# Kernel tuning notes

Measured on AMD Instinct MI355X. Metric: run time of the kernel, lower is better.

The kernel has to match this reference:

```python
import jax, jax.numpy as jnp
import numpy as np

LATENT_DIM = 64
CONTEXT_DIM = 128
NUM_LAYERS = 5
NUM_BINS = 8
HIDDEN = 256
TAIL_BOUND = 5.0
MIN_BIN_W = 1e-3
MIN_BIN_H = 1e-3
MIN_DERIV = 1e-3
BATCH = 32768


def setup_inputs() -> dict:
    key = jax.random.key(0)
    ks = jax.random.split(key, 8)
    D, C, L, H = LATENT_DIM, CONTEXT_DIM, NUM_LAYERS, HIDDEN
    out_dim = D * (3 * NUM_BINS - 1)  # 64*23 = 1472
    n_tri = D * (D - 1) // 2  # 2016
    s = 0.05
    return {
        "inputs": jax.random.normal(ks[0], (BATCH, D), jnp.float32) * 2.0,
        "context": jax.random.normal(ks[1], (BATCH, C), jnp.float32),
        "W1": jax.random.normal(ks[2], (L, C, H), jnp.float32) * s,
        "b1": jnp.zeros((L, H), jnp.float32),
        "W2": jax.random.normal(ks[3], (L, H, H), jnp.float32) * s,
        "b2": jnp.zeros((L, H), jnp.float32),
        "W3": jax.random.normal(ks[4], (L, H, out_dim), jnp.float32) * s,
        "b3": jnp.zeros((L, out_dim), jnp.float32),
        "lu_bias": jnp.zeros((L, D), jnp.float32),
        "lower_entries": jax.random.normal(ks[5], (L, n_tri), jnp.float32) * s,
        "upper_entries": jax.random.normal(ks[6], (L, n_tri), jnp.float32) * s,
        "upper_diag": jax.random.normal(ks[7], (L, D), jnp.float32) * s,
    }


def _unconstrained_rqs(x, uw, uh, ud):
    """Rational-quadratic spline with linear tails (nflows semantics).
    x: [B, D]; uw/uh: [B, D, NUM_BINS]; ud: [B, D, NUM_BINS-1].
    Returns (y [B,D], logabsdet [B,D])."""
    Bnd = TAIL_BOUND
    nb = NUM_BINS
    inside = (x >= -Bnd) & (x <= Bnd)
    # pad unnormalized derivatives so boundary derivative == 1
    const = float(np.log(np.exp(1.0 - MIN_DERIV) - 1.0))
    ud = jnp.pad(ud, ((0, 0), (0, 0), (1, 1)), constant_values=const)  # [B,D,nb+1]

    w = jax.nn.softmax(uw, axis=-1)
    w = MIN_BIN_W + (1.0 - MIN_BIN_W * nb) * w
    cumw = jnp.concatenate(
        [jnp.zeros(w.shape[:-1] + (1,), w.dtype), jnp.cumsum(w, axis=-1)], axis=-1)
    cumw = 2.0 * Bnd * cumw - Bnd
    cumw = cumw.at[..., 0].set(-Bnd).at[..., -1].set(Bnd)
    widths = cumw[..., 1:] - cumw[..., :-1]

    h = jax.nn.softmax(uh, axis=-1)
    h = MIN_BIN_H + (1.0 - MIN_BIN_H * nb) * h
    cumh = jnp.concatenate(
        [jnp.zeros(h.shape[:-1] + (1,), h.dtype), jnp.cumsum(h, axis=-1)], axis=-1)
    cumh = 2.0 * Bnd * cumh - Bnd
    cumh = cumh.at[..., 0].set(-Bnd).at[..., -1].set(Bnd)
    heights = cumh[..., 1:] - cumh[..., :-1]

    derivs = MIN_DERIV + jax.nn.softplus(ud)  # [B,D,nb+1]
    delta = heights / widths                  # [B,D,nb]

    xc = jnp.clip(x, -Bnd, Bnd)
    # searchsorted: sum(x >= bin_edges) - 1, clipped to valid bin range
    idx = jnp.clip(jnp.sum(xc[..., None] >= cumw, axis=-1) - 1, 0, nb - 1)[..., None]
    g = lambda a: jnp.take_along_axis(a, idx, axis=-1)[..., 0]

    in_cw = g(cumw)
    in_w = g(widths)
    in_ch = g(cumh)
    in_h = g(heights)
    in_delta = g(delta)
    in_d = g(derivs)
    in_d1 = g(derivs[..., 1:])

    theta = (xc - in_cw) / in_w
    tomt = theta * (1.0 - theta)
    numer = in_h * (in_delta * theta * theta + in_d * tomt)
    denom = in_delta + (in_d + in_d1 - 2.0 * in_delta) * tomt
    out = in_ch + numer / denom
    dnum = in_delta * in_delta * (
        in_d1 * theta * theta + 2.0 * in_delta * tomt + in_d * (1.0 - theta) ** 2)
    ld = jnp.log(dnum) - 2.0 * jnp.log(denom)

    return jnp.where(inside, out, x), jnp.where(inside, ld, 0.0)


def _lu_forward(x, lower_e, upper_e, udiag, bias):
    """nflows LULinear: y = L @ (U @ x) + b, logabsdet = sum(log diag(U))."""
    D = x.shape[-1]
    li = jnp.tril_indices(D, -1)
    ui = jnp.triu_indices(D, 1)
    Lm = jnp.eye(D, dtype=x.dtype).at[li].set(lower_e)
    diag = jax.nn.softplus(udiag) + 1e-3
    Um = jnp.zeros((D, D), x.dtype).at[ui].set(upper_e) + jnp.diag(diag)
    y = x @ Um.T
    y = y @ Lm.T + bias
    return y, jnp.sum(jnp.log(diag))


def reference(inputs, context, W1, b1, W2, b2, W3, b3,
              lu_bias, lower_entries, upper_entries, upper_diag):
    x = inputs
    logdet = jnp.zeros(x.shape[0], x.dtype)
    for l in range(NUM_LAYERS):
        # conditioning net (mask=ones => net sees only context)
        hh = jax.nn.relu(context @ W1[l] + b1[l])
        hh = jax.nn.relu(hh @ W2[l] + b2[l])
        params = (hh @ W3[l] + b3[l]).reshape(x.shape[0], LATENT_DIM, 3 * NUM_BINS - 1)
        uw = params[..., :NUM_BINS]
        uh = params[..., NUM_BINS:2 * NUM_BINS]
        ud = params[..., 2 * NUM_BINS:]
        x, ld = _unconstrained_rqs(x, uw, uh, ud)
        logdet = logdet + jnp.sum(ld, axis=-1)
        x, lld = _lu_forward(x, lower_entries[l], upper_entries[l],
                             upper_diag[l], lu_bias[l])
        logdet = logdet + lld
    base = -0.5 * jnp.sum(x * x, axis=-1) - 0.5 * LATENT_DIM * float(np.log(2.0 * np.pi))
    return base + logdet
```

## Files before the change

kernel.cpp:

```cpp
#include <hip/hip_runtime.h>
#include <hip/hip_bf16.h>
#include <math.h>

#define D 64
#define CDIM 128
#define NL 5
#define NB 8
#define HID 256
#define ODIM 1472
#define PPD 23
#define PPDP 24
#define NPAD 1536
#define NTRI 2016
#define BATCH 32768
#define CHUNK 8192

typedef unsigned short u16;
typedef __attribute__((ext_vector_type(8))) short bf16x8;
typedef __attribute__((ext_vector_type(8))) unsigned short u16x8;
typedef __attribute__((ext_vector_type(4))) float f32x4;
typedef __attribute__((ext_vector_type(8))) float f32x8;

__device__ __forceinline__ float softplusf(float x) {
    return fmaxf(x, 0.0f) + log1pf(__expf(-fabsf(x)));
}
__device__ __forceinline__ float softplus_fast(float x) {
    return fmaxf(x, 0.0f) + __logf(1.0f + __expf(-fabsf(x)));
}
__device__ __forceinline__ float frcp(float x) { return __builtin_amdgcn_rcpf(x); }
__device__ __forceinline__ u16 f2bf(float f) {
    __hip_bfloat16 h = __float2bfloat16(f);
    return *reinterpret_cast<u16*>(&h);
}
__device__ __forceinline__ float bf2f(u16 u) {
    return __uint_as_float(((unsigned int)u) << 16);
}

__device__ __forceinline__ void gload16(const u16* g, const u16* s) {
    __builtin_amdgcn_global_load_lds(
        (const __attribute__((address_space(1))) unsigned int*)(unsigned long long)(uintptr_t)g,
        (__attribute__((address_space(3))) unsigned int*)(unsigned int)(uintptr_t)s,
        16, 0, 0);
}

__device__ __forceinline__ int xcd_swz(int bid, int nwg) {
    int q = nwg >> 3, r = nwg & 7;
    int xcd = bid & 7, idx = bid >> 3;
    return (xcd < r ? xcd * (q + 1) : r * (q + 1) + (xcd - r) * q) + idx;
}

__global__ void cvt_ctx(const float* __restrict__ c, u16* __restrict__ o) {
    int i = blockIdx.x * 256 + threadIdx.x;
    if (i < BATCH * CDIM / 4) {
        float4 v = reinterpret_cast<const float4*>(c)[i];
        unsigned lo = (unsigned)f2bf(v.x) | ((unsigned)f2bf(v.y) << 16);
        unsigned hi = (unsigned)f2bf(v.z) | ((unsigned)f2bf(v.w) << 16);
        uint2 pv; pv.x = lo; pv.y = hi;
        reinterpret_cast<uint2*>(o)[i] = pv;
    }
}

template<int MAP>
__global__ __launch_bounds__(256) void transpose_prep(
    const float* __restrict__ in, u16* __restrict__ out, int R, int C, int Cout)
{
    __shared__ u16 tile[32][33];
    const int l = blockIdx.z;
    const int c0 = blockIdx.x * 32, r0 = blockIdx.y * 32;
    const int tx = threadIdx.x & 31, ty = threadIdx.x >> 5;
    const float* inl = in + (size_t)l * R * C;
#pragma unroll
    for (int i = 0; i < 4; ++i) {
        int r = r0 + ty * 4 + i;
        int cc = c0 + tx;
        int src = cc;
        if (MAP) { int dd = cc / PPDP, pp = cc % PPDP; src = (pp < PPD) ? dd * PPD + pp : -1; }
        u16 v = 0;
        if (src >= 0) v = f2bf(inl[(size_t)r * C + src]);
        tile[ty * 4 + i][tx] = v;
    }
    __syncthreads();
    u16* outl = out + (size_t)l * Cout * R;
#pragma unroll
    for (int i = 0; i < 4; ++i) {
        int cc = c0 + ty * 4 + i;
        outl[(size_t)cc * R + r0 + tx] = tile[tx][ty * 4 + i];
    }
}

__global__ void prep_b3(const float* __restrict__ b3, float* __restrict__ b3p) {
    int i = blockIdx.x * 256 + threadIdx.x;
    if (i < NL * NPAD) {
        int n = i % NPAD; int l = i / NPAD;
        int dd = n / PPDP, p = n % PPDP;
        b3p[i] = (p < PPD) ? b3[l * ODIM + dd * PPD + p] : 0.0f;
    }
}

__global__ void lu_prep(const float* __restrict__ lower_e,
                        const float* __restrict__ upper_e,
                        const float* __restrict__ udiag,
                        float* __restrict__ At, float* __restrict__ lu_const) {
    int l = blockIdx.x;
    int t = threadIdx.x;
    __shared__ float Ls[D * D];
    __shared__ float Us[D * D];
    __shared__ float red[4];
    for (int idx = t; idx < D * D; idx += 256) {
        int i = idx >> 6, j = idx & 63;
        float lv;
        if (i == j)      lv = 1.0f;
        else if (i > j)  lv = lower_e[l * NTRI + (i * (i - 1)) / 2 + j];
        else             lv = 0.0f;
        Ls[idx] = lv;
        float uv;
        if (i == j)      uv = softplusf(udiag[l * D + i]) + 0.001f;
        else if (j > i)  uv = upper_e[l * NTRI + i * (D - 1) - (i * (i - 1)) / 2 + (j - i - 1)];
        else             uv = 0.0f;
        Us[idx] = uv;
    }
    __syncthreads();
    for (int idx = t; idx < D * D; idx += 256) {
        int i = idx >> 6, j = idx & 63;
        float acc = 0.0f;
        int km = min(i, j);
        for (int k = 0; k <= km; ++k) acc += Ls[i * D + k] * Us[k * D + j];
        At[(l * D + j) * D + i] = acc;
    }
    if (l == 0) {
        float s = 0.0f;
        for (int i = t; i < NL * D; i += 256)
            s += __logf(softplusf(udiag[i]) + 0.001f);
#pragma unroll
        for (int off = 32; off; off >>= 1) s += __shfl_xor(s, off);
        if ((t & 63) == 0) red[t >> 6] = s;
        __syncthreads();
        if (t == 0) lu_const[0] = red[0] + red[1] + red[2] + red[3];
    }
}

__global__ void init_kernel(const float* __restrict__ inp, float* __restrict__ x,
                            float* __restrict__ logdet) {
    int i = blockIdx.x * 256 + threadIdx.x;
    if (i < BATCH * D) x[i] = inp[i];
    if (i < BATCH) logdet[i] = 0.0f;
}

template<int RELU>
__global__ __launch_bounds__(256) void gemm_bf16(
    const u16* __restrict__ A, const u16* __restrict__ Bt,
    const float* __restrict__ bias, u16* __restrict__ Cv,
    int N, int K, int ncol)
{
    __shared__ u16 lds[16384];
    const int t = threadIdx.x;
    const int w = t >> 6, l = t & 63;
    const int wm = w >> 1, wn = w & 1;
    const int wg = xcd_swz(blockIdx.x, gridDim.x);
    const size_t m0 = (size_t)(wg / ncol) * 128;
    const int n0 = (wg % ncol) * 128;
    const int lrow = l & 15, lk = l >> 4;
    const int srow = l >> 3, sslot = l & 7;

    f32x4 acc[4][4] = {};

    for (int k0 = 0; k0 < K; k0 += 64) {
#pragma unroll
        for (int q = 0; q < 4; ++q) {
            int c = q * 4 + w;
            int row = c * 8 + srow;
            int slog = sslot ^ (row & 7);
            gload16(A + (m0 + row) * K + k0 + slog * 8, &lds[c * 512]);
        }
#pragma unroll
        for (int q = 0; q < 4; ++q) {
            int c = q * 4 + w;
            int row = c * 8 + srow;
            int slog = sslot ^ (row & 7);
            gload16(Bt + (size_t)(n0 + row) * K + k0 + slog * 8, &lds[8192 + c * 512]);
        }
        __syncthreads();
#pragma unroll
        for (int ks = 0; ks < 2; ++ks) {
            bf16x8 a[4], b[4];
#pragma unroll
            for (int mf = 0; mf < 4; ++mf) {
                int row = wm * 64 + mf * 16 + lrow;
                int slot = (ks * 4 + lk) ^ (row & 7);
                a[mf] = *(const bf16x8*)&lds[row * 64 + slot * 8];
            }
#pragma unroll
            for (int nf = 0; nf < 4; ++nf) {
                int row = wn * 64 + nf * 16 + lrow;
                int slot = (ks * 4 + lk) ^ (row & 7);
                b[nf] = *(const bf16x8*)&lds[8192 + row * 64 + slot * 8];
            }
#pragma unroll
            for (int mf = 0; mf < 4; ++mf)
#pragma unroll
                for (int nf = 0; nf < 4; ++nf)
                    acc[mf][nf] = __builtin_amdgcn_mfma_f32_16x16x32_bf16(
                        a[mf], b[nf], acc[mf][nf], 0, 0, 0);
        }
        __syncthreads();
    }

    {
        u16* region = &lds[w * 4096];
#pragma unroll
        for (int nf = 0; nf < 4; ++nf) {
            float bv = bias[n0 + wn * 64 + nf * 16 + lrow];
#pragma unroll
            for (int mf = 0; mf < 4; ++mf) {
#pragma unroll
                for (int i = 0; i < 4; ++i) {
                    float v = acc[mf][nf][i] + bv;
                    if (RELU) v = fmaxf(v, 0.0f);
                    unsigned b = (unsigned)f2bf(v);
                    unsigned o = __shfl_xor(b, 1);
                    if (!(lrow & 1)) {
                        int r = mf * 16 + lk * 4 + i;
                        int slot = (nf << 1) | (lrow >> 3);
                        int dw = r * 32 + ((slot ^ (r & 7)) << 2) + ((lrow & 7) >> 1);
                        *reinterpret_cast<unsigned*>(&region[dw * 2]) = b | (o << 16);
                    }
                }
            }
        }
#pragma unroll
        for (int s = 0; s < 8; ++s) {
            int r = s * 8 + (l >> 3);
            int slot = (l & 7) ^ (r & 7);
            bf16x8 vv = *(const bf16x8*)&region[r * 64 + slot * 8];
            *(bf16x8*)(Cv + (m0 + wm * 64 + r) * N + n0 + wn * 64 + 8 * (l & 7)) = vv;
        }
    }
}

__device__ __forceinline__ f32x8 cumb(f32x8 p) {
    float m = fmaxf(fmaxf(fmaxf(p[0], p[1]), fmaxf(p[2], p[3])),
                    fmaxf(fmaxf(p[4], p[5]), fmaxf(p[6], p[7])));
    f32x8 e;
    float s = 0.0f;
#pragma unroll
    for (int i = 0; i < 8; ++i) { e[i] = __expf(p[i] - m); s += e[i]; }
    float tt = 0.992f * frcp(s);
    f32x8 c;
    float run = 0.0f;
#pragma unroll
    for (int i = 0; i < 7; ++i) {
        run = fmaf(tt, e[i], run + 0.001f);
        c[i] = fmaf(10.0f, run, -5.0f);
    }
    c[7] = 5.0f;
    return c;
}

__device__ __forceinline__ void rqs_v(float xv, f32x8 uw, f32x8 uh, f32x8 ud,
                                      float& yo, float& ldo) {
    f32x8 cw = cumb(uw);
    f32x8 ch = cumb(uh);
    f32x8 dv;
#pragma unroll
    for (int i = 0; i < 7; ++i) dv[i] = 0.001f + softplus_fast(ud[i]);
    float xc = fminf(fmaxf(xv, -5.0f), 5.0f);
    float icw = -5.0f, icw1 = cw[0], ich = -5.0f, ich1 = ch[0];
    float d0 = 1.0f, d1 = dv[0];
#pragma unroll
    for (int k = 1; k < 8; ++k) {
        bool sel = (xc >= cw[k - 1]);
        icw  = sel ? cw[k - 1] : icw;
        icw1 = sel ? cw[k]     : icw1;
        ich  = sel ? ch[k - 1] : ich;
        ich1 = sel ? ch[k]     : ich1;
        d0   = sel ? dv[k - 1] : d0;
        d1   = sel ? ((k < 7) ? dv[k] : 1.0f) : d1;
    }
    float iw  = icw1 - icw;
    float ih  = ich1 - ich;
    float riw = frcp(iw);
    float dlt = ih * riw;
    float th  = (xc - icw) * riw;
    float omt = 1.0f - th;
    float tomt = th * omt;
    float numer = ih * (dlt * th * th + d0 * tomt);
    float den = dlt + (d0 + d1 - 2.0f * dlt) * tomt;
    float rden = frcp(den);
    float outv = ich + numer * rden;
    float dnum = dlt * dlt * (d1 * th * th + 2.0f * dlt * tomt + d0 * omt * omt);
    float ld = __logf(dnum * rden * rden);
    bool inside = (xv >= -5.0f) && (xv <= 5.0f);
    yo  = inside ? outv : xv;
    ldo = inside ? ld : 0.0f;
}

__global__ __launch_bounds__(512) void spline_lu_kernel(
    const u16* __restrict__ params,
    const float* __restrict__ At, const float* __restrict__ lu_bias,
    float* __restrict__ x, float* __restrict__ logdet,
    int l, int row_base)
{
    __shared__ float y_s[8 * D];
    const int t = threadIdx.x;
    const int d = t & 63, g = t >> 6;
    const size_t crow = (size_t)blockIdx.x * 8 + g;
    const size_t grow = (size_t)row_base + crow;

    const u16x8* pp = (const u16x8*)(params + crow * NPAD + d * PPDP);
    u16x8 q0 = pp[0], q1 = pp[1], q2 = pp[2];
    f32x8 uw, uh, ud;
#pragma unroll
    for (int j = 0; j < 8; ++j) {
        uw[j] = bf2f(q0[j]);
        uh[j] = bf2f(q1[j]);
        ud[j] = bf2f(q2[j]);
    }
    float xv = x[grow * D + d];
    float y, ld;
    rqs_v(xv, uw, uh, ud, y, ld);
    y_s[g * D + d] = y;
#pragma unroll
    for (int off = 32; off; off >>= 1) ld += __shfl_xor(ld, off);
    if (d == 0) logdet[grow] += ld;
    __syncthreads();

    float acc = lu_bias[l * D + d];
    const float* ap = At + (size_t)l * D * D + d;
#pragma unroll 8
    for (int j = 0; j < D; ++j)
        acc = fmaf(y_s[g * D + j], ap[j * D], acc);
    x[grow * D + d] = acc;
}

__global__ void final_kernel(const float* __restrict__ x,
                             const float* __restrict__ logdet,
                             const float* __restrict__ lu_const,
                             float* __restrict__ out) {
    int t = threadIdx.x;
    int b = blockIdx.x * 4 + (t >> 6);
    int d = t & 63;
    float v = x[(size_t)b * D + d];
    float s = v * v;
#pragma unroll
    for (int off = 32; off; off >>= 1) s += __shfl_xor(s, off);
    if (d == 0)
        out[b] = logdet[b] + lu_const[0] - 0.5f * s - 0.5f * 64.0f * 1.8378770664093453f;
}

extern "C" void kernel_launch(void* const* d_in, const int* in_sizes, int n_in,
                              void* d_out, int out_size, void* d_ws, size_t ws_size,
                              hipStream_t stream) {
    const float* inputs  = (const float*)d_in[0];
    const float* context = (const float*)d_in[1];
    const float* W1      = (const float*)d_in[2];
    const float* b1      = (const float*)d_in[3];
    const float* W2      = (const float*)d_in[4];
    const float* b2      = (const float*)d_in[5];
    const float* W3      = (const float*)d_in[6];
    const float* b3      = (const float*)d_in[7];
    const float* lu_bias = (const float*)d_in[8];
    const float* lower_e = (const float*)d_in[9];
    const float* upper_e = (const float*)d_in[10];
    const float* udiag   = (const float*)d_in[11];
    float* out = (float*)d_out;

    char* p = (char*)d_ws;
    auto alloc = [&](size_t bytes) { void* r = p; p += (bytes + 255) & ~(size_t)255; return r; };
    float* x        = (float*)alloc((size_t)BATCH * D * 4);
    float* logdet   = (float*)alloc((size_t)BATCH * 4);
    float* At       = (float*)alloc((size_t)NL * D * D * 4);
    float* lu_const = (float*)alloc(256);
    u16*   ctx_bf   = (u16*)alloc((size_t)BATCH * CDIM * 2);
    u16*   hh1      = (u16*)alloc((size_t)BATCH * HID * 2);
    u16*   hh2      = (u16*)alloc((size_t)BATCH * HID * 2);
    u16*   W1t      = (u16*)alloc((size_t)NL * HID * CDIM * 2);
    u16*   W2t      = (u16*)alloc((size_t)NL * HID * HID * 2);
    u16*   W3t      = (u16*)alloc((size_t)NL * NPAD * HID * 2);
    float* b3p      = (float*)alloc((size_t)NL * NPAD * 4);

    size_t used = (size_t)(p - (char*)d_ws);
    int chunk = (ws_size - used >= (size_t)BATCH * NPAD * 2 + 256) ? BATCH : CHUNK;
    u16* paramsB = (u16*)alloc((size_t)chunk * NPAD * 2);

    cvt_ctx<<<(BATCH * CDIM / 4 + 255) / 256, 256, 0, stream>>>(context, ctx_bf);
    transpose_prep<0><<<dim3(HID / 32, CDIM / 32, NL), 256, 0, stream>>>(
        W1, W1t, CDIM, HID, HID);
    transpose_prep<0><<<dim3(HID / 32, HID / 32, NL), 256, 0, stream>>>(
        W2, W2t, HID, HID, HID);
    transpose_prep<1><<<dim3(NPAD / 32, HID / 32, NL), 256, 0, stream>>>(
        W3, W3t, HID, ODIM, NPAD);
    prep_b3<<<(NL * NPAD + 255) / 256, 256, 0, stream>>>(b3, b3p);
    lu_prep<<<NL, 256, 0, stream>>>(lower_e, upper_e, udiag, At, lu_const);
    init_kernel<<<(BATCH * D + 255) / 256, 256, 0, stream>>>(inputs, x, logdet);

    for (int l = 0; l < NL; ++l) {
        gemm_bf16<1><<<(BATCH / 128) * 2, 256, 0, stream>>>(
            ctx_bf, W1t + (size_t)l * HID * CDIM, b1 + l * HID, hh1, HID, CDIM, 2);
        gemm_bf16<1><<<(BATCH / 128) * 2, 256, 0, stream>>>(
            hh1, W2t + (size_t)l * HID * HID, b2 + l * HID, hh2, HID, HID, 2);
        for (int c = 0; c < BATCH / chunk; ++c) {
            gemm_bf16<0><<<(chunk / 128) * (NPAD / 128), 256, 0, stream>>>(
                hh2 + (size_t)c * chunk * HID, W3t + (size_t)l * NPAD * HID,
                b3p + l * NPAD, paramsB, NPAD, HID, NPAD / 128);
            spline_lu_kernel<<<chunk / 8, 512, 0, stream>>>(
                paramsB, At, lu_bias, x, logdet, l, c * chunk);
        }
    }
    final_kernel<<<BATCH / 4, 256, 0, stream>>>(x, logdet, lu_const, out);
}
```

Baseline: 590.8 us.

## Batch conditioning MLP GEMMs across layers and use direct nontemporal epilogue stores

```diff
diff --git a/kernel.cpp b/kernel.cpp
--- a/kernel.cpp
+++ b/kernel.cpp
@@ -146,13 +146,18 @@
     if (i < BATCH) logdet[i] = 0.0f;
 }
 
-template<int RELU>
+template<int RELU, int NT>
 __global__ __launch_bounds__(256) void gemm_bf16(
-    const u16* __restrict__ A, const u16* __restrict__ Bt,
-    const float* __restrict__ bias, u16* __restrict__ Cv,
-    int N, int K, int ncol)
+    const u16* __restrict__ A0, const u16* __restrict__ Bt0,
+    const float* __restrict__ bias0, u16* __restrict__ Cv0,
+    int N, int K, int ncol, size_t sA, size_t sB, size_t sb, size_t sC)
 {
     __shared__ u16 lds[16384];
+    const int ly = blockIdx.y;
+    const u16* A = A0 + (size_t)ly * sA;
+    const u16* Bt = Bt0 + (size_t)ly * sB;
+    const float* bias = bias0 + (size_t)ly * sb;
+    u16* Cv = Cv0 + (size_t)ly * sC;
     const int t = threadIdx.x;
     const int w = t >> 6, l = t & 63;
     const int wm = w >> 1, wn = w & 1;
@@ -204,35 +209,21 @@
         }
         __syncthreads();
     }
-
-    {
-        u16* region = &lds[w * 4096];
-#pragma unroll
-        for (int nf = 0; nf < 4; ++nf) {
-            float bv = bias[n0 + wn * 64 + nf * 16 + lrow];
-#pragma unroll
-            for (int mf = 0; mf < 4; ++mf) {
-#pragma unroll
-                for (int i = 0; i < 4; ++i) {
-                    float v = acc[mf][nf][i] + bv;
-                    if (RELU) v = fmaxf(v, 0.0f);
-                    unsigned b = (unsigned)f2bf(v);
-                    unsigned o = __shfl_xor(b, 1);
-                    if (!(lrow & 1)) {
-                        int r = mf * 16 + lk * 4 + i;
-                        int slot = (nf << 1) | (lrow >> 3);
-                        int dw = r * 32 + ((slot ^ (r & 7)) << 2) + ((lrow & 7) >> 1);
-                        *reinterpret_cast<unsigned*>(&region[dw * 2]) = b | (o << 16);
-                    }
-                }
+#pragma unroll
+    for (int nf = 0; nf < 4; ++nf) {
+        int col = n0 + wn * 64 + nf * 16 + lrow;
+        float bv = bias[col];
+#pragma unroll
+        for (int mf = 0; mf < 4; ++mf) {
+            size_t rbase = m0 + wm * 64 + mf * 16 + lk * 4;
+#pragma unroll
+            for (int i = 0; i < 4; ++i) {
+                float v = acc[mf][nf][i] + bv;
+                if (RELU) v = fmaxf(v, 0.0f);
+                u16 bb = f2bf(v);
+                if (NT) __builtin_nontemporal_store(bb, Cv + (rbase + i) * N + col);
+                else    Cv[(rbase + i) * N + col] = bb;
             }
-        }
-#pragma unroll
-        for (int s = 0; s < 8; ++s) {
-            int r = s * 8 + (l >> 3);
-            int slot = (l & 7) ^ (r & 7);
-            bf16x8 vv = *(const bf16x8*)&region[r * 64 + slot * 8];
-            *(bf16x8*)(Cv + (m0 + wm * 64 + r) * N + n0 + wn * 64 + 8 * (l & 7)) = vv;
         }
     }
 }
@@ -371,8 +362,8 @@
     float* At       = (float*)alloc((size_t)NL * D * D * 4);
     float* lu_const = (float*)alloc(256);
     u16*   ctx_bf   = (u16*)alloc((size_t)BATCH * CDIM * 2);
-    u16*   hh1      = (u16*)alloc((size_t)BATCH * HID * 2);
-    u16*   hh2      = (u16*)alloc((size_t)BATCH * HID * 2);
+    u16*   hh1      = (u16*)alloc((size_t)NL * BATCH * HID * 2);
+    u16*   hh2      = (u16*)alloc((size_t)NL * BATCH * HID * 2);
     u16*   W1t      = (u16*)alloc((size_t)NL * HID * CDIM * 2);
     u16*   W2t      = (u16*)alloc((size_t)NL * HID * HID * 2);
     u16*   W3t      = (u16*)alloc((size_t)NL * NPAD * HID * 2);
@@ -393,15 +384,21 @@
     lu_prep<<<NL, 256, 0, stream>>>(lower_e, upper_e, udiag, At, lu_const);
     init_kernel<<<(BATCH * D + 255) / 256, 256, 0, stream>>>(inputs, x, logdet);
 
+    dim3 gmlp((BATCH / 128) * 2, NL);
+    gemm_bf16<1, 0><<<gmlp, 256, 0, stream>>>(
+        ctx_bf, W1t, b1, hh1, HID, CDIM, 2,
+        0, (size_t)HID * CDIM, HID, (size_t)BATCH * HID);
+    gemm_bf16<1, 0><<<gmlp, 256, 0, stream>>>(
+        hh1, W2t, b2, hh2, HID, HID, 2,
+        (size_t)BATCH * HID, (size_t)HID * HID, HID, (size_t)BATCH * HID);
+
     for (int l = 0; l < NL; ++l) {
-        gemm_bf16<1><<<(BATCH / 128) * 2, 256, 0, stream>>>(
-            ctx_bf, W1t + (size_t)l * HID * CDIM, b1 + l * HID, hh1, HID, CDIM, 2);
-        gemm_bf16<1><<<(BATCH / 128) * 2, 256, 0, stream>>>(
-            hh1, W2t + (size_t)l * HID * HID, b2 + l * HID, hh2, HID, HID, 2);
         for (int c = 0; c < BATCH / chunk; ++c) {
-            gemm_bf16<0><<<(chunk / 128) * (NPAD / 128), 256, 0, stream>>>(
-                hh2 + (size_t)c * chunk * HID, W3t + (size_t)l * NPAD * HID,
-                b3p + l * NPAD, paramsB, NPAD, HID, NPAD / 128);
+            dim3 g3((chunk / 128) * (NPAD / 128), 1);
+            gemm_bf16<0, 1><<<g3, 256, 0, stream>>>(
+                hh2 + (size_t)l * BATCH * HID + (size_t)c * chunk * HID,
+                W3t + (size_t)l * NPAD * HID, b3p + (size_t)l * NPAD,
+                paramsB, NPAD, HID, NPAD / 128, 0, 0, 0, 0);
             spline_lu_kernel<<<chunk / 8, 512, 0, stream>>>(
                 paramsB, At, lu_bias, x, logdet, l, c * chunk);
         }
```

Result: slower. 823.6 us (+39.4%).
